# Kernel optimization log

Hardware: AMD Instinct MI355X
Metric: run time of the kernel (lower is better)

## Reference

```python
import jax, jax.numpy as jnp
import numpy as np

B, N, H, HEADS = 8, 1024, 512, 4  # batch graphs, nodes/graph, graph_hsz, attention heads
R = 64  # relations per graph (passthrough)


def setup_inputs() -> dict:
    key = jax.random.key(0)
    k1, k2, k3, k4, k5, k6, k7 = jax.random.split(key, 7)
    adjs = jax.random.randint(k1, (B, N, N), 0, 2, dtype=jnp.int32)  # 0 => masked
    nodes = jax.random.normal(k2, (B, N, H), dtype=jnp.float32)
    triples = jax.random.normal(k3, (B, R, H), dtype=jnp.float32)   # unused in gat path
    relations = jax.random.normal(k4, (B, R, H), dtype=jnp.float32)  # passthrough
    node_num = jnp.full((B,), N, dtype=jnp.int32)  # all graphs full => no padding branch
    s = 1.0 / np.sqrt(H)
    Wq = (jax.random.normal(k5, (H, H), dtype=jnp.float32) * s)
    Wk = (jax.random.normal(k6, (H, H), dtype=jnp.float32) * s)
    Wv = (jax.random.normal(k7, (H, H), dtype=jnp.float32) * s)
    return {"adjs": adjs, "triples": triples, "nodes": nodes, "node_num": node_num,
            "relations": relations, "Wq": Wq, "Wk": Wk, "Wv": Wv}


def reference(adjs, triples, nodes, node_num, relations, Wq, Wk, Wv):
    b, n, h = nodes.shape
    dk = h // HEADS
    scale = 1.0 / jnp.sqrt(jnp.float32(h))  # torch divides by sqrt(key_dim)=sqrt(H)

    def to_heads(x, W):  # [B,N,H] -> [B,heads,N,dk]; matches split(dim=-1)+stack
        return (x @ W).reshape(b, n, HEADS, dk).transpose(0, 2, 1, 3)

    Q = to_heads(nodes, Wq)
    K = to_heads(nodes, Wk)
    V = to_heads(nodes, Wv)
    att = jnp.einsum('bhnd,bhmd->bhnm', Q, K) * scale
    att = jnp.where((adjs == 0)[:, None, :, :], -jnp.inf, att)
    p = jax.nn.softmax(att, axis=-1)  # dropout_p = blockdrop = 0.0 => identity
    out = jnp.einsum('bhnm,bhmd->bhnd', p, V)
    out = out.transpose(0, 2, 1, 3).reshape(b, n, h)  # concat heads along feature dim
    out = jax.nn.relu(out)
    return (out, relations)
```

## Files before the change

kernel.cpp:

```cpp
#include <hip/hip_runtime.h>
#include <stdint.h>

typedef __attribute__((ext_vector_type(4))) float f32x4;
typedef __attribute__((ext_vector_type(16))) float f32x16;
typedef __attribute__((ext_vector_type(8))) short bf16x8;
typedef unsigned long long ull;

#define GLB_AS const __attribute__((address_space(1)))
#define LDS_AS __attribute__((address_space(3)))

__device__ __forceinline__ short f2bf(float f) {
    union { float f; unsigned u; } x; x.f = f;
    unsigned r = x.u + 0x7FFFu + ((x.u >> 16) & 1u);
    return (short)(r >> 16);
}

__global__ void k_pre(const float* __restrict__ nodes, short* __restrict__ nodes_bf,
                      const float* __restrict__ Wq, const float* __restrict__ Wk,
                      const float* __restrict__ Wv, short* __restrict__ WT,
                      const int* __restrict__ adjs, unsigned* __restrict__ packed) {
    int bi = blockIdx.x, tid = threadIdx.x;
    if (bi < 2048) {
        int i = (bi * 256 + tid) * 8;
        float4 a = *(const float4*)(nodes + i);
        float4 b = *(const float4*)(nodes + i + 4);
        bf16x8 v;
        v[0] = f2bf(a.x); v[1] = f2bf(a.y); v[2] = f2bf(a.z); v[3] = f2bf(a.w);
        v[4] = f2bf(b.x); v[5] = f2bf(b.y); v[6] = f2bf(b.z); v[7] = f2bf(b.w);
        *(bf16x8*)(nodes_bf + i) = v;
    } else if (bi < 5120) {
        int g = (bi - 2048) * 256 + tid;
        int j = g >> 9, k = g & 511;
        int w = j >> 9, n = j & 511;
        const float* W = (w == 0) ? Wq : (w == 1) ? Wk : Wv;
        WT[g] = f2bf(W[k * 512 + n]);
    } else {
        int g = (bi - 5120) * 256 + tid;
        int wv = g >> 6, lane = g & 63;
        ull m = __ballot(adjs[(size_t)wv * 64 + lane] != 0);
        if (lane == 0) *(ull*)(packed + (size_t)wv * 2) = m;
    }
}

__global__ __launch_bounds__(256) void k_gemm_qkv(const short* __restrict__ A,
                                                  const short* __restrict__ WT,
                                                  short* __restrict__ C) {
    __shared__ short Asm[2][128 * 32];
    __shared__ short Bsm[2][128 * 32];
    const int tid = threadIdx.x;
    const int l = tid & 63, w = tid >> 6;
    const int wr = w >> 1, wc = w & 1;
    const int c16 = l & 15, g = l >> 4;
    const int wg = blockIdx.x;
    const int swz = (wg & 7) * 96 + (wg >> 3);
    const int row0 = (swz / 12) * 128, n0 = (swz % 12) * 128;
    f32x4 acc[4][4] = {};

    auto stage = [&](int kt, int bsel) {
        const int k0 = kt * 32;
#pragma unroll
        for (int i = 0; i < 2; ++i) {
            int ch = tid + 256 * i;
            int r = ch >> 2, gc = ch & 3;
            __builtin_amdgcn_global_load_lds((GLB_AS unsigned*)(A + (row0 + r) * 512 + k0 + 8 * gc),
                                             (LDS_AS unsigned*)(&Asm[bsel][ch * 8]), 16, 0, 0);
            __builtin_amdgcn_global_load_lds((GLB_AS unsigned*)(WT + (n0 + r) * 512 + k0 + 8 * gc),
                                             (LDS_AS unsigned*)(&Bsm[bsel][ch * 8]), 16, 0, 0);
        }
    };

    stage(0, 0);
    asm volatile("s_waitcnt vmcnt(0)" ::: "memory");
    __syncthreads();

    for (int kt = 0; kt < 16; ++kt) {
        const int cur = kt & 1;
        if (kt < 15) stage(kt + 1, cur ^ 1);
        bf16x8 af[4], bfr[4];
#pragma unroll
        for (int mf = 0; mf < 4; ++mf)
            af[mf] = *(const bf16x8*)&Asm[cur][(wr * 64 + mf * 16 + c16) * 32 + 8 * g];
#pragma unroll
        for (int nf = 0; nf < 4; ++nf)
            bfr[nf] = *(const bf16x8*)&Bsm[cur][(wc * 64 + nf * 16 + c16) * 32 + 8 * g];
#pragma unroll
        for (int mf = 0; mf < 4; ++mf)
#pragma unroll
            for (int nf = 0; nf < 4; ++nf)
                acc[mf][nf] = __builtin_amdgcn_mfma_f32_16x16x32_bf16(af[mf], bfr[nf], acc[mf][nf], 0, 0, 0);
        asm volatile("s_waitcnt vmcnt(0)" ::: "memory");
        __syncthreads();
    }
#pragma unroll
    for (int mf = 0; mf < 4; ++mf)
#pragma unroll
        for (int nf = 0; nf < 4; ++nf) {
            const float cs = (n0 + wc * 64 + nf * 16 < 512) ? 0.06375872022286384f : 1.0f;
#pragma unroll
            for (int r = 0; r < 4; ++r) {
                int row = row0 + wr * 64 + mf * 16 + 4 * g + r;
                int col = n0 + wc * 64 + nf * 16 + c16;
                C[row * 1536 + col] = f2bf(acc[mf][nf][r] * cs);
            }
        }
}

__global__ __launch_bounds__(256) void k_mid(const short* __restrict__ QKV, short* __restrict__ Vt,
                                             const float* __restrict__ rel_in, float* __restrict__ rel_out) {
    __shared__ short tile[64 * 65];
    const int bi = blockIdx.x, t = threadIdx.x;
    if (bi >= 1024) {
        int i = ((bi - 1024) * 256 + t) * 4;
        *(float4*)(rel_out + i) = *(const float4*)(rel_in + i);
        return;
    }
    const int b = bi >> 7, n0 = ((bi >> 3) & 15) * 64, d0 = (bi & 7) * 64;
#pragma unroll
    for (int i = 0; i < 16; ++i) {
        int idx = t + 256 * i;
        int nn = idx >> 6, dd = idx & 63;
        tile[nn * 65 + dd] = QKV[(b * 1024 + n0 + nn) * 1536 + 1024 + d0 + dd];
    }
    __syncthreads();
#pragma unroll
    for (int i = 0; i < 16; ++i) {
        int idx = t + 256 * i;
        int dd = idx >> 6, nn = idx & 63;
        Vt[(b * 512 + d0 + dd) * 1024 + n0 + nn] = tile[nn * 65 + dd];
    }
}

__global__ __launch_bounds__(256, 2) void k_attn(const short* __restrict__ QKV, const short* __restrict__ Vt,
                                                 const unsigned* __restrict__ packed, float* __restrict__ out) {
    __shared__ short Ksm[2][64 * 128];
    __shared__ short Vsm[2][128 * 64];
    const int bh = blockIdx.x;
    const int b = bh >> 2, h = bh & 3;
    const int q0 = blockIdx.y * 128;
    const int tid = threadIdx.x, l = tid & 63, wid = tid >> 6;
    const int l31 = l & 31, hi = l >> 5;
    const int qw = q0 + wid * 32;

    bf16x8 aq[8];
    const short* Qb = QKV + (size_t)(b * 1024 + qw + l31) * 1536 + h * 128;
#pragma unroll
    for (int kk = 0; kk < 8; ++kk)
        aq[kk] = *(const bf16x8*)(Qb + kk * 16 + hi * 8);

    f32x16 acc[4] = {};
    float l_lane = 0.f;

    const short* Kbase = QKV + (size_t)(b * 1024) * 1536 + 512 + h * 128;
    const short* Vtbase = Vt + (size_t)(b * 512 + h * 128) * 1024;
    const ull* adjq = (const ull*)packed + (size_t)(b * 1024 + qw + l31) * 16;

    auto stage = [&](int t, int bsel) {
        const int m0 = t * 64;
#pragma unroll
        for (int i = 0; i < 4; ++i) {
            int ch = tid + 256 * i;
            int mr = ch >> 4, gc = ch & 15;
            int gs = gc ^ (mr & 7);
            __builtin_amdgcn_global_load_lds((GLB_AS unsigned*)(Kbase + (size_t)(m0 + mr) * 1536 + 8 * gs),
                                             (LDS_AS unsigned*)(&Ksm[bsel][ch * 8]), 16, 0, 0);
        }
#pragma unroll
        for (int i = 0; i < 4; ++i) {
            int ch = tid + 256 * i;
            int dr = ch >> 3, gc = ch & 7;
            int gs = gc ^ (dr & 7);
            __builtin_amdgcn_global_load_lds((GLB_AS unsigned*)(Vtbase + (size_t)dr * 1024 + m0 + 8 * gs),
                                             (LDS_AS unsigned*)(&Vsm[bsel][ch * 8]), 16, 0, 0);
        }
    };

    ull mcur = adjq[0], mnxt = 0;
    stage(0, 0);
    asm volatile("s_waitcnt vmcnt(0)" ::: "memory");
    __builtin_amdgcn_s_barrier();

    for (int t = 0; t < 16; ++t) {
        const int cur = t & 1;
        if (t < 15) {
            mnxt = adjq[t + 1];
            stage(t + 1, cur ^ 1);
        }

        f32x16 s[2] = {};
        __builtin_amdgcn_s_setprio(1);
#pragma unroll
        for (int kk = 0; kk < 8; ++kk)
#pragma unroll
            for (int mm = 0; mm < 2; ++mm) {
                const int row = mm * 32 + l31;
                const int chunk = (2 * kk + hi) ^ (row & 7);
                bf16x8 ak = *(const bf16x8*)&Ksm[cur][row * 128 + chunk * 8];
                s[mm] = __builtin_amdgcn_mfma_f32_32x32x16_bf16(ak, aq[kk], s[mm], 0, 0, 0);
            }
        __builtin_amdgcn_s_setprio(0);

        unsigned pk[2][4][2];
#pragma unroll
        for (int mm = 0; mm < 2; ++mm) {
            const unsigned mshift = (unsigned)(mcur >> (32 * mm + 4 * hi));
#pragma unroll
            for (int j = 0; j < 4; ++j) {
                float p[4];
#pragma unroll
                for (int r = 0; r < 4; ++r) {
                    float e = __builtin_amdgcn_exp2f(s[mm][4 * j + r]);
                    p[r] = ((mshift >> (8 * j + r)) & 1u) ? e : 0.f;
                    l_lane += p[r];
                }
                asm("v_cvt_pk_bf16_f32 %0, %1, %2" : "=v"(pk[mm][j][0]) : "v"(p[0]), "v"(p[1]));
                asm("v_cvt_pk_bf16_f32 %0, %1, %2" : "=v"(pk[mm][j][1]) : "v"(p[2]), "v"(p[3]));
            }
        }

        union fragu { unsigned u[4]; bf16x8 v; };
        fragu frag[4];
#pragma unroll
        for (int mm = 0; mm < 2; ++mm)
#pragma unroll
            for (int kh = 0; kh < 2; ++kh) {
                unsigned a0 = pk[mm][2 * kh][0], a1 = pk[mm][2 * kh][1];
                unsigned b0 = pk[mm][2 * kh + 1][0], b1 = pk[mm][2 * kh + 1][1];
                unsigned rx0 = (unsigned)__shfl_xor((int)a0, 32);
                unsigned rx1 = (unsigned)__shfl_xor((int)a1, 32);
                unsigned rx2 = (unsigned)__shfl_xor((int)b0, 32);
                unsigned rx3 = (unsigned)__shfl_xor((int)b1, 32);
                fragu f;
                f.u[0] = hi ? rx2 : a0;
                f.u[1] = hi ? rx3 : a1;
                f.u[2] = hi ? b0 : rx0;
                f.u[3] = hi ? b1 : rx1;
                frag[2 * mm + kh] = f;
            }

        if (t < 15) { asm volatile("s_waitcnt vmcnt(9)" ::: "memory"); }
        else        { asm volatile("s_waitcnt vmcnt(0)" ::: "memory"); }
        __builtin_amdgcn_s_barrier();

        __builtin_amdgcn_s_setprio(1);
#pragma unroll
        for (int ks = 0; ks < 4; ++ks)
#pragma unroll
            for (int dd = 0; dd < 4; ++dd) {
                const int row = dd * 32 + l31;
                const int chunk = (2 * ks + hi) ^ (row & 7);
                bf16x8 bv = *(const bf16x8*)&Vsm[cur][row * 64 + chunk * 8];
                acc[dd] = __builtin_amdgcn_mfma_f32_32x32x16_bf16(frag[ks].v, bv, acc[dd], 0, 0, 0);
            }
        __builtin_amdgcn_s_setprio(0);

        mcur = mnxt;

        if (t < 15) {
            asm volatile("s_waitcnt vmcnt(4)" ::: "memory");
            __builtin_amdgcn_s_barrier();
        }
    }

    l_lane += __shfl_xor(l_lane, 32);
    float inv_own = 1.f / l_lane;
    float iv[16];
#pragma unroll
    for (int j = 0; j < 4; ++j)
#pragma unroll
        for (int r = 0; r < 4; ++r)
            iv[4 * j + r] = __shfl(inv_own, r + 8 * j + 4 * hi);

#pragma unroll
    for (int dd = 0; dd < 4; ++dd)
#pragma unroll
        for (int j = 0; j < 4; ++j)
#pragma unroll
            for (int r = 0; r < 4; ++r) {
                int q32 = r + 8 * j + 4 * hi;
                float o = fmaxf(acc[dd][4 * j + r] * iv[4 * j + r], 0.f);
                out[(size_t)(b * 1024 + qw + q32) * 512 + h * 128 + dd * 32 + l31] = o;
            }
}

extern "C" void kernel_launch(void* const* d_in, const int* in_sizes, int n_in,
                              void* d_out, int out_size, void* d_ws, size_t ws_size,
                              hipStream_t stream) {
    const int*   adjs      = (const int*)d_in[0];
    const float* nodes     = (const float*)d_in[2];
    const float* relations = (const float*)d_in[4];
    const float* Wq        = (const float*)d_in[5];
    const float* Wk        = (const float*)d_in[6];
    const float* Wv        = (const float*)d_in[7];

    char* ws = (char*)d_ws;
    short* nodes_bf   = (short*)(ws);
    short* WT         = (short*)(ws + 8388608);
    short* QKV        = (short*)(ws + 9961472);
    short* Vt         = (short*)(ws + 35127296);
    unsigned* adjpack = (unsigned*)(ws + 43515904);

    float* out     = (float*)d_out;
    float* out_rel = out + 4194304;

    k_pre<<<dim3(37888), dim3(256), 0, stream>>>(nodes, nodes_bf, Wq, Wk, Wv, WT, adjs, adjpack);
    k_gemm_qkv<<<dim3(768), dim3(256), 0, stream>>>(nodes_bf, WT, QKV);
    k_mid<<<dim3(1280), dim3(256), 0, stream>>>(QKV, Vt, relations, out_rel);
    k_attn<<<dim3(32, 8), dim3(256), 0, stream>>>(QKV, Vt, adjpack, out);
}
```

Measured before the change: 86.64 us.

## Split attention key range across two blocks and combine partial sums

The attention kernel now splits the 1024 keys into two halves along a new grid dimension, doubling the block count from 256 to 512 so the GPU's compute units are better filled. The first half writes unnormalized fp32 partial outputs into the output buffer, the second half writes bf16 partials to workspace, and each writes its row sums. A new combine kernel adds the partials, normalizes and applies ReLU. Softmax needs no max shift because no max is subtracted, so partials add directly. This costs an extra launch and extra global traffic, and the second half's partial is rounded to bf16. The K swizzle also changes from 8-way to 16-way.

```diff
diff --git a/kernel.cpp b/kernel.cpp
--- a/kernel.cpp
+++ b/kernel.cpp
@@ -13,6 +13,10 @@
     union { float f; unsigned u; } x; x.f = f;
     unsigned r = x.u + 0x7FFFu + ((x.u >> 16) & 1u);
     return (short)(r >> 16);
+}
+__device__ __forceinline__ float bf2f(short s) {
+    union { unsigned u; float f; } x; x.u = ((unsigned)(unsigned short)s) << 16;
+    return x.f;
 }
 
 __global__ void k_pre(const float* __restrict__ nodes, short* __restrict__ nodes_bf,
@@ -131,15 +135,19 @@
 }
 
 __global__ __launch_bounds__(256, 2) void k_attn(const short* __restrict__ QKV, const short* __restrict__ Vt,
-                                                 const unsigned* __restrict__ packed, float* __restrict__ out) {
+                                                 const unsigned* __restrict__ packed,
+                                                 float* __restrict__ o0, short* __restrict__ o1,
+                                                 float* __restrict__ lpart) {
     __shared__ short Ksm[2][64 * 128];
     __shared__ short Vsm[2][128 * 64];
     const int bh = blockIdx.x;
     const int b = bh >> 2, h = bh & 3;
     const int q0 = blockIdx.y * 128;
+    const int mh = blockIdx.z;
     const int tid = threadIdx.x, l = tid & 63, wid = tid >> 6;
     const int l31 = l & 31, hi = l >> 5;
     const int qw = q0 + wid * 32;
+    const int mbase = mh * 512;
 
     bf16x8 aq[8];
     const short* Qb = QKV + (size_t)(b * 1024 + qw + l31) * 1536 + h * 128;
@@ -152,15 +160,15 @@
 
     const short* Kbase = QKV + (size_t)(b * 1024) * 1536 + 512 + h * 128;
     const short* Vtbase = Vt + (size_t)(b * 512 + h * 128) * 1024;
-    const ull* adjq = (const ull*)packed + (size_t)(b * 1024 + qw + l31) * 16;
+    const ull* adjq = (const ull*)packed + (size_t)(b * 1024 + qw + l31) * 16 + mh * 8;
 
     auto stage = [&](int t, int bsel) {
-        const int m0 = t * 64;
+        const int m0 = mbase + t * 64;
 #pragma unroll
         for (int i = 0; i < 4; ++i) {
             int ch = tid + 256 * i;
             int mr = ch >> 4, gc = ch & 15;
-            int gs = gc ^ (mr & 7);
+            int gs = gc ^ (mr & 15);
             __builtin_amdgcn_global_load_lds((GLB_AS unsigned*)(Kbase + (size_t)(m0 + mr) * 1536 + 8 * gs),
                                              (LDS_AS unsigned*)(&Ksm[bsel][ch * 8]), 16, 0, 0);
         }
@@ -179,9 +187,9 @@
     asm volatile("s_waitcnt vmcnt(0)" ::: "memory");
     __builtin_amdgcn_s_barrier();
 
-    for (int t = 0; t < 16; ++t) {
+    for (int t = 0; t < 8; ++t) {
         const int cur = t & 1;
-        if (t < 15) {
+        if (t < 7) {
             mnxt = adjq[t + 1];
             stage(t + 1, cur ^ 1);
         }
@@ -193,13 +201,14 @@
 #pragma unroll
             for (int mm = 0; mm < 2; ++mm) {
                 const int row = mm * 32 + l31;
-                const int chunk = (2 * kk + hi) ^ (row & 7);
+                const int chunk = (2 * kk + hi) ^ (row & 15);
                 bf16x8 ak = *(const bf16x8*)&Ksm[cur][row * 128 + chunk * 8];
                 s[mm] = __builtin_amdgcn_mfma_f32_32x32x16_bf16(ak, aq[kk], s[mm], 0, 0, 0);
             }
         __builtin_amdgcn_s_setprio(0);
 
         unsigned pk[2][4][2];
+        float lt = 0.f;
 #pragma unroll
         for (int mm = 0; mm < 2; ++mm) {
             const unsigned mshift = (unsigned)(mcur >> (32 * mm + 4 * hi));
@@ -210,12 +219,13 @@
                 for (int r = 0; r < 4; ++r) {
                     float e = __builtin_amdgcn_exp2f(s[mm][4 * j + r]);
                     p[r] = ((mshift >> (8 * j + r)) & 1u) ? e : 0.f;
-                    l_lane += p[r];
                 }
+                lt += (p[0] + p[1]) + (p[2] + p[3]);
                 asm("v_cvt_pk_bf16_f32 %0, %1, %2" : "=v"(pk[mm][j][0]) : "v"(p[0]), "v"(p[1]));
                 asm("v_cvt_pk_bf16_f32 %0, %1, %2" : "=v"(pk[mm][j][1]) : "v"(p[2]), "v"(p[3]));
             }
         }
+        l_lane += lt;
 
         union fragu { unsigned u[4]; bf16x8 v; };
         fragu frag[4];
@@ -237,8 +247,8 @@
                 frag[2 * mm + kh] = f;
             }
 
-        if (t < 15) { asm volatile("s_waitcnt vmcnt(9)" ::: "memory"); }
-        else        { asm volatile("s_waitcnt vmcnt(0)" ::: "memory"); }
+        if (t < 7) { asm volatile("s_waitcnt vmcnt(9)" ::: "memory"); }
+        else       { asm volatile("s_waitcnt vmcnt(0)" ::: "memory"); }
         __builtin_amdgcn_s_barrier();
 
         __builtin_amdgcn_s_setprio(1);
@@ -255,31 +265,61 @@
 
         mcur = mnxt;
 
-        if (t < 15) {
+        if (t < 7) {
             asm volatile("s_waitcnt vmcnt(4)" ::: "memory");
             __builtin_amdgcn_s_barrier();
         }
     }
 
     l_lane += __shfl_xor(l_lane, 32);
-    float inv_own = 1.f / l_lane;
-    float iv[16];
-#pragma unroll
-    for (int j = 0; j < 4; ++j)
-#pragma unroll
-        for (int r = 0; r < 4; ++r)
-            iv[4 * j + r] = __shfl(inv_own, r + 8 * j + 4 * hi);
-
-#pragma unroll
-    for (int dd = 0; dd < 4; ++dd)
-#pragma unroll
-        for (int j = 0; j < 4; ++j)
-#pragma unroll
-            for (int r = 0; r < 4; ++r) {
-                int q32 = r + 8 * j + 4 * hi;
-                float o = fmaxf(acc[dd][4 * j + r] * iv[4 * j + r], 0.f);
-                out[(size_t)(b * 1024 + qw + q32) * 512 + h * 128 + dd * 32 + l31] = o;
-            }
+
+    if (mh == 0) {
+#pragma unroll
+        for (int dd = 0; dd < 4; ++dd)
+#pragma unroll
+            for (int j = 0; j < 4; ++j)
+#pragma unroll
+                for (int r = 0; r < 4; ++r) {
+                    int q32 = r + 8 * j + 4 * hi;
+                    o0[(size_t)(b * 1024 + qw + q32) * 512 + h * 128 + dd * 32 + l31] = acc[dd][4 * j + r];
+                }
+    } else {
+#pragma unroll
+        for (int dd = 0; dd < 4; ++dd)
+#pragma unroll
+            for (int j = 0; j < 4; ++j)
+#pragma unroll
+                for (int r = 0; r < 4; ++r) {
+                    int q32 = r + 8 * j + 4 * hi;
+                    o1[(size_t)(b * 1024 + qw + q32) * 512 + h * 128 + dd * 32 + l31] = f2bf(acc[dd][4 * j + r]);
+                }
+    }
+    if (hi == 0)
+        lpart[mh * 32768 + (b * 4 + h) * 1024 + qw + l31] = l_lane;
+}
+
+__global__ void k_combine(float* __restrict__ out, const short* __restrict__ o1,
+                          const float* __restrict__ lp) {
+    int i = (blockIdx.x * 256 + threadIdx.x) * 8;
+    int b = i >> 19;
+    int q = (i >> 9) & 1023;
+    int h = (i >> 7) & 3;
+    int lidx = (b * 4 + h) * 1024 + q;
+    float inv = 1.f / (lp[lidx] + lp[32768 + lidx]);
+    float4 a0 = *(const float4*)(out + i);
+    float4 a1 = *(const float4*)(out + i + 4);
+    bf16x8 c = *(const bf16x8*)(o1 + i);
+    float4 r0, r1;
+    r0.x = fmaxf((a0.x + bf2f(c[0])) * inv, 0.f);
+    r0.y = fmaxf((a0.y + bf2f(c[1])) * inv, 0.f);
+    r0.z = fmaxf((a0.z + bf2f(c[2])) * inv, 0.f);
+    r0.w = fmaxf((a0.w + bf2f(c[3])) * inv, 0.f);
+    r1.x = fmaxf((a1.x + bf2f(c[4])) * inv, 0.f);
+    r1.y = fmaxf((a1.y + bf2f(c[5])) * inv, 0.f);
+    r1.z = fmaxf((a1.z + bf2f(c[6])) * inv, 0.f);
+    r1.w = fmaxf((a1.w + bf2f(c[7])) * inv, 0.f);
+    *(float4*)(out + i) = r0;
+    *(float4*)(out + i + 4) = r1;
 }
 
 extern "C" void kernel_launch(void* const* d_in, const int* in_sizes, int n_in,
@@ -298,6 +338,8 @@
     short* QKV        = (short*)(ws + 9961472);
     short* Vt         = (short*)(ws + 35127296);
     unsigned* adjpack = (unsigned*)(ws + 43515904);
+    short* opart1 = (short*)(ws);
+    float* lpart  = (float*)(ws + 8388608);
 
     float* out     = (float*)d_out;
     float* out_rel = out + 4194304;
@@ -305,5 +347,6 @@
     k_pre<<<dim3(37888), dim3(256), 0, stream>>>(nodes, nodes_bf, Wq, Wk, Wv, WT, adjs, adjpack);
     k_gemm_qkv<<<dim3(768), dim3(256), 0, stream>>>(nodes_bf, WT, QKV);
     k_mid<<<dim3(1280), dim3(256), 0, stream>>>(QKV, Vt, relations, out_rel);
-    k_attn<<<dim3(32, 8), dim3(256), 0, stream>>>(QKV, Vt, adjpack, out);
-}
+    k_attn<<<dim3(32, 8, 2), dim3(256), 0, stream>>>(QKV, Vt, adjpack, out, opart1, lpart);
+    k_combine<<<dim3(2048), dim3(256), 0, stream>>>(out, opart1, lpart);
+}
```

New measurement: 84.72 us. 2.2% less time.

## Split attention key range across two wave groups and read V directly in fragment layout

Applied to the files above, without the earlier changes.

The attention kernel now launches 512 threads per block. Two groups of four waves each process half of the key sequence, and their partial outputs and row sums are combined through shared memory at the end. V is rewritten by the transpose kernel into an MFMA-fragment-friendly layout, so each lane loads its B operand straight from global memory instead of staging V through LDS, which frees LDS for a larger swizzled K buffer per group. The aim is more waves in flight per block and less LDS traffic and barrier waiting. The cost is an extra LDS reduction epilogue, global-latency-bound V loads inside the loop, and full vmcnt(0) waits every iteration.

```diff
diff --git a/kernel.cpp b/kernel.cpp
--- a/kernel.cpp
+++ b/kernel.cpp
@@ -105,7 +105,7 @@
         }
 }
 
-__global__ __launch_bounds__(256) void k_mid(const short* __restrict__ QKV, short* __restrict__ Vt,
+__global__ __launch_bounds__(256) void k_mid(const short* __restrict__ QKV, short* __restrict__ Vt2,
                                              const float* __restrict__ rel_in, float* __restrict__ rel_out) {
     __shared__ short tile[64 * 65];
     const int bi = blockIdx.x, t = threadIdx.x;
@@ -123,23 +123,33 @@
     }
     __syncthreads();
 #pragma unroll
-    for (int i = 0; i < 16; ++i) {
-        int idx = t + 256 * i;
-        int dd = idx >> 6, nn = idx & 63;
-        Vt[(b * 512 + d0 + dd) * 1024 + n0 + nn] = tile[nn * 65 + dd];
-    }
-}
-
-__global__ __launch_bounds__(256, 2) void k_attn(const short* __restrict__ QKV, const short* __restrict__ Vt,
+    for (int i = 0; i < 2; ++i) {
+        int c = t + 256 * i;
+        int dd = c >> 3, nl = (c & 7) * 8;
+        int dg = d0 + dd;
+        int h = dg >> 7, dh = dg & 127;
+        bf16x8 v;
+#pragma unroll
+        for (int e = 0; e < 8; ++e)
+            v[e] = tile[(nl + e) * 65 + dd];
+        *(bf16x8*)(Vt2 + ((((size_t)(b * 4 + h)) * 128 + ((n0 + nl) >> 3)) * 128 + dh) * 8) = v;
+    }
+}
+
+__global__ __launch_bounds__(512, 1) void k_attn(const short* __restrict__ QKV, const short* __restrict__ Vt2,
                                                  const unsigned* __restrict__ packed, float* __restrict__ out) {
-    __shared__ short Ksm[2][64 * 128];
-    __shared__ short Vsm[2][128 * 64];
+    __shared__ char smem[66560];
+    short* Ksm = (short*)smem;
+    float* Osh = (float*)smem;
+    float* lsh = (float*)(smem + 65536);
     const int bh = blockIdx.x;
     const int b = bh >> 2, h = bh & 3;
     const int q0 = blockIdx.y * 128;
     const int tid = threadIdx.x, l = tid & 63, wid = tid >> 6;
+    const int mg = wid >> 2, wq = wid & 3;
+    const int gt = tid & 255;
     const int l31 = l & 31, hi = l >> 5;
-    const int qw = q0 + wid * 32;
+    const int qw = q0 + wq * 32;
 
     bf16x8 aq[8];
     const short* Qb = QKV + (size_t)(b * 1024 + qw + l31) * 1536 + h * 128;
@@ -151,55 +161,58 @@
     float l_lane = 0.f;
 
     const short* Kbase = QKV + (size_t)(b * 1024) * 1536 + 512 + h * 128;
-    const short* Vtbase = Vt + (size_t)(b * 512 + h * 128) * 1024;
-    const ull* adjq = (const ull*)packed + (size_t)(b * 1024 + qw + l31) * 16;
-
-    auto stage = [&](int t, int bsel) {
-        const int m0 = t * 64;
+    const short* V2b = Vt2 + (size_t)(b * 4 + h) * 131072;
+    const ull* adjq = (const ull*)packed + (size_t)(b * 1024 + qw + l31) * 16 + mg * 8;
+
+    auto stageK = [&](int t, int bsel) {
+        const int m0 = mg * 512 + t * 64;
+        short* dst = Ksm + (mg * 2 + bsel) * 8192;
 #pragma unroll
         for (int i = 0; i < 4; ++i) {
-            int ch = tid + 256 * i;
+            int ch = gt + 256 * i;
             int mr = ch >> 4, gc = ch & 15;
-            int gs = gc ^ (mr & 7);
+            int gs = gc ^ (mr & 15);
             __builtin_amdgcn_global_load_lds((GLB_AS unsigned*)(Kbase + (size_t)(m0 + mr) * 1536 + 8 * gs),
-                                             (LDS_AS unsigned*)(&Ksm[bsel][ch * 8]), 16, 0, 0);
-        }
-#pragma unroll
-        for (int i = 0; i < 4; ++i) {
-            int ch = tid + 256 * i;
-            int dr = ch >> 3, gc = ch & 7;
-            int gs = gc ^ (dr & 7);
-            __builtin_amdgcn_global_load_lds((GLB_AS unsigned*)(Vtbase + (size_t)dr * 1024 + m0 + 8 * gs),
-                                             (LDS_AS unsigned*)(&Vsm[bsel][ch * 8]), 16, 0, 0);
+                                             (LDS_AS unsigned*)(dst + ch * 8), 16, 0, 0);
         }
     };
 
     ull mcur = adjq[0], mnxt = 0;
-    stage(0, 0);
+    stageK(0, 0);
     asm volatile("s_waitcnt vmcnt(0)" ::: "memory");
     __builtin_amdgcn_s_barrier();
 
-    for (int t = 0; t < 16; ++t) {
+    for (int t = 0; t < 8; ++t) {
         const int cur = t & 1;
-        if (t < 15) {
+        if (t < 7) {
+            stageK(t + 1, cur ^ 1);
             mnxt = adjq[t + 1];
-            stage(t + 1, cur ^ 1);
-        }
-
-        f32x16 s[2] = {};
+        }
+        const int mc0 = mg * 64 + t * 8;
+        bf16x8 bv[2][4];
+#pragma unroll
+        for (int ks = 0; ks < 2; ++ks)
+#pragma unroll
+            for (int dd = 0; dd < 4; ++dd)
+                bv[ks][dd] = *(const bf16x8*)(V2b + (((size_t)(mc0 + 2 * ks + hi)) * 128 + dd * 32 + l31) * 8);
+
+        const short* Kb = Ksm + (mg * 2 + cur) * 8192;
+        f32x16 s[2];
+        s[0] = (f32x16)0.f; s[1] = (f32x16)0.f;
         __builtin_amdgcn_s_setprio(1);
 #pragma unroll
         for (int kk = 0; kk < 8; ++kk)
 #pragma unroll
             for (int mm = 0; mm < 2; ++mm) {
                 const int row = mm * 32 + l31;
-                const int chunk = (2 * kk + hi) ^ (row & 7);
-                bf16x8 ak = *(const bf16x8*)&Ksm[cur][row * 128 + chunk * 8];
+                const int chunk = (2 * kk + hi) ^ (row & 15);
+                bf16x8 ak = *(const bf16x8*)&Kb[row * 128 + chunk * 8];
                 s[mm] = __builtin_amdgcn_mfma_f32_32x32x16_bf16(ak, aq[kk], s[mm], 0, 0, 0);
             }
         __builtin_amdgcn_s_setprio(0);
 
         unsigned pk[2][4][2];
+        float lt = 0.f;
 #pragma unroll
         for (int mm = 0; mm < 2; ++mm) {
             const unsigned mshift = (unsigned)(mcur >> (32 * mm + 4 * hi));
@@ -210,17 +223,18 @@
                 for (int r = 0; r < 4; ++r) {
                     float e = __builtin_amdgcn_exp2f(s[mm][4 * j + r]);
                     p[r] = ((mshift >> (8 * j + r)) & 1u) ? e : 0.f;
-                    l_lane += p[r];
                 }
+                lt += (p[0] + p[1]) + (p[2] + p[3]);
                 asm("v_cvt_pk_bf16_f32 %0, %1, %2" : "=v"(pk[mm][j][0]) : "v"(p[0]), "v"(p[1]));
                 asm("v_cvt_pk_bf16_f32 %0, %1, %2" : "=v"(pk[mm][j][1]) : "v"(p[2]), "v"(p[3]));
             }
         }
+        l_lane += lt;
 
         union fragu { unsigned u[4]; bf16x8 v; };
-        fragu frag[4];
-#pragma unroll
-        for (int mm = 0; mm < 2; ++mm)
+#pragma unroll
+        for (int mm = 0; mm < 2; ++mm) {
+            fragu frag[2];
 #pragma unroll
             for (int kh = 0; kh < 2; ++kh) {
                 unsigned a0 = pk[mm][2 * kh][0], a1 = pk[mm][2 * kh][1];
@@ -234,52 +248,70 @@
                 f.u[1] = hi ? rx3 : a1;
                 f.u[2] = hi ? b0 : rx0;
                 f.u[3] = hi ? b1 : rx1;
-                frag[2 * mm + kh] = f;
-            }
-
-        if (t < 15) { asm volatile("s_waitcnt vmcnt(9)" ::: "memory"); }
-        else        { asm volatile("s_waitcnt vmcnt(0)" ::: "memory"); }
+                frag[kh] = f;
+            }
+            __builtin_amdgcn_s_setprio(1);
+#pragma unroll
+            for (int kh = 0; kh < 2; ++kh) {
+                const int ksl = 2 * mm + kh;
+#pragma unroll
+                for (int dd = 0; dd < 4; ++dd) {
+                    bf16x8 bvv;
+                    if (ksl < 2) bvv = bv[ksl][dd];
+                    else         bvv = *(const bf16x8*)(V2b + (((size_t)(mc0 + 2 * ksl + hi)) * 128 + dd * 32 + l31) * 8);
+                    acc[dd] = __builtin_amdgcn_mfma_f32_32x32x16_bf16(frag[kh].v, bvv, acc[dd], 0, 0, 0);
+                }
+            }
+            __builtin_amdgcn_s_setprio(0);
+        }
+
+        mcur = mnxt;
+        asm volatile("s_waitcnt vmcnt(0)" ::: "memory");
         __builtin_amdgcn_s_barrier();
-
-        __builtin_amdgcn_s_setprio(1);
-#pragma unroll
-        for (int ks = 0; ks < 4; ++ks)
-#pragma unroll
-            for (int dd = 0; dd < 4; ++dd) {
-                const int row = dd * 32 + l31;
-                const int chunk = (2 * ks + hi) ^ (row & 7);
-                bf16x8 bv = *(const bf16x8*)&Vsm[cur][row * 64 + chunk * 8];
-                acc[dd] = __builtin_amdgcn_mfma_f32_32x32x16_bf16(frag[ks].v, bv, acc[dd], 0, 0, 0);
-            }
-        __builtin_amdgcn_s_setprio(0);
-
-        mcur = mnxt;
-
-        if (t < 15) {
-            asm volatile("s_waitcnt vmcnt(4)" ::: "memory");
-            __builtin_amdgcn_s_barrier();
-        }
     }
 
     l_lane += __shfl_xor(l_lane, 32);
-    float inv_own = 1.f / l_lane;
-    float iv[16];
-#pragma unroll
-    for (int j = 0; j < 4; ++j)
-#pragma unroll
-        for (int r = 0; r < 4; ++r)
-            iv[4 * j + r] = __shfl(inv_own, r + 8 * j + 4 * hi);
-
-#pragma unroll
-    for (int dd = 0; dd < 4; ++dd)
+    if (hi == 0) lsh[mg * 128 + wq * 32 + l31] = l_lane;
+
+    if (mg == 1) {
+#pragma unroll
+        for (int dd = 0; dd < 4; ++dd)
+#pragma unroll
+            for (int j = 0; j < 4; ++j)
+#pragma unroll
+                for (int r = 0; r < 4; ++r) {
+                    int qrow = wq * 32 + r + 8 * j + 4 * hi;
+                    Osh[qrow * 128 + dd * 32 + l31] = acc[dd][4 * j + r];
+                }
+    }
+    __syncthreads();
+    if (mg == 0) {
+        float inv[4][2];
 #pragma unroll
         for (int j = 0; j < 4; ++j)
 #pragma unroll
+            for (int r2 = 0; r2 < 2; ++r2) {
+                inv[j][r2] = 0.f;
+            }
+        float invq[16];
+#pragma unroll
+        for (int j = 0; j < 4; ++j)
+#pragma unroll
             for (int r = 0; r < 4; ++r) {
-                int q32 = r + 8 * j + 4 * hi;
-                float o = fmaxf(acc[dd][4 * j + r] * iv[4 * j + r], 0.f);
-                out[(size_t)(b * 1024 + qw + q32) * 512 + h * 128 + dd * 32 + l31] = o;
-            }
+                int qrow = wq * 32 + r + 8 * j + 4 * hi;
+                invq[4 * j + r] = 1.f / (lsh[qrow] + lsh[128 + qrow]);
+            }
+#pragma unroll
+        for (int dd = 0; dd < 4; ++dd)
+#pragma unroll
+            for (int j = 0; j < 4; ++j)
+#pragma unroll
+                for (int r = 0; r < 4; ++r) {
+                    int qrow = wq * 32 + r + 8 * j + 4 * hi;
+                    float o = (acc[dd][4 * j + r] + Osh[qrow * 128 + dd * 32 + l31]) * invq[4 * j + r];
+                    out[(size_t)(b * 1024 + q0 + qrow) * 512 + h * 128 + dd * 32 + l31] = fmaxf(o, 0.f);
+                }
+    }
 }
 
 extern "C" void kernel_launch(void* const* d_in, const int* in_sizes, int n_in,
@@ -296,7 +328,7 @@
     short* nodes_bf   = (short*)(ws);
     short* WT         = (short*)(ws + 8388608);
     short* QKV        = (short*)(ws + 9961472);
-    short* Vt         = (short*)(ws + 35127296);
+    short* Vt2        = (short*)(ws + 35127296);
     unsigned* adjpack = (unsigned*)(ws + 43515904);
 
     float* out     = (float*)d_out;
@@ -304,6 +336,6 @@
 
     k_pre<<<dim3(37888), dim3(256), 0, stream>>>(nodes, nodes_bf, Wq, Wk, Wv, WT, adjs, adjpack);
     k_gemm_qkv<<<dim3(768), dim3(256), 0, stream>>>(nodes_bf, WT, QKV);
-    k_mid<<<dim3(1280), dim3(256), 0, stream>>>(QKV, Vt, relations, out_rel);
-    k_attn<<<dim3(32, 8), dim3(256), 0, stream>>>(QKV, Vt, adjpack, out);
-}
+    k_mid<<<dim3(1280), dim3(256), 0, stream>>>(QKV, Vt2, relations, out_rel);
+    k_attn<<<dim3(32, 8), dim3(512), 0, stream>>>(QKV, Vt2, adjpack, out);
+}
```

New measurement: 82.15 us. 1.05x faster.
